# Kernel optimization log

Hardware: AMD Instinct MI355X
Metric: run time of the kernel (lower is better)

## Reference

```python
import jax, jax.numpy as jnp
import numpy as np

N, E, IN_DIM, OUT_DIM, HEADS = 50000, 800000, 128, 64, 2
NEG_SLOPE = 0.2  # DGL GATConv default leaky_relu slope


def setup_inputs() -> dict:
    key = jax.random.key(0)
    ks = jax.random.split(key, 11)
    p = lambda k, shape: jax.random.normal(k, shape, jnp.float32) * 0.05
    return dict(
        feature=jax.random.normal(ks[0], (N, IN_DIM), jnp.float32),
        src=jax.random.randint(ks[1], (E,), 0, N, jnp.int32),
        dst=jax.random.randint(ks[2], (E,), 0, N, jnp.int32),
        W1=p(ks[3], (IN_DIM, HEADS * OUT_DIM)),
        al1=p(ks[4], (HEADS, OUT_DIM)),
        ar1=p(ks[5], (HEADS, OUT_DIM)),
        b1=p(ks[6], (HEADS * OUT_DIM,)),
        W2=p(ks[7], (HEADS * OUT_DIM, OUT_DIM)),
        al2=p(ks[8], (1, OUT_DIM)),
        ar2=p(ks[9], (1, OUT_DIM)),
        b2=p(ks[10], (OUT_DIM,)),
    )


def gat_conv(x, W, al, ar, b, src, dst, n_nodes):
    # DGL GATConv (eval mode): fc -> per-node attn halves -> edge leaky_relu
    # -> edge-softmax grouped by dst -> scatter-weighted sum -> + bias
    H, D = al.shape
    h = (x @ W).reshape(n_nodes, H, D)               # [N,H,D]
    el = jnp.einsum('nhd,hd->nh', h, al)             # [N,H]
    er = jnp.einsum('nhd,hd->nh', h, ar)             # [N,H]
    e = jax.nn.leaky_relu(el[src] + er[dst], NEG_SLOPE)  # [E,H]
    m = jax.ops.segment_max(e, dst, num_segments=n_nodes)
    m = jnp.where(jnp.isfinite(m), m, 0.0)           # guard isolated dst nodes
    ex = jnp.exp(e - m[dst])                         # [E,H]
    s = jax.ops.segment_sum(ex, dst, num_segments=n_nodes)
    alpha = ex / s[dst]                              # edge-softmax weights
    out = jax.ops.segment_sum(alpha[:, :, None] * h[src], dst,
                              num_segments=n_nodes)  # [N,H,D]
    return out + b.reshape(H, D)


def reference(feature, src, dst, W1, al1, ar1, b1, W2, al2, ar2, b2):
    h1 = jax.nn.elu(gat_conv(feature, W1, al1, ar1, b1, src, dst, N))  # [N,2,D]
    h2 = gat_conv(h1.reshape(N, -1), W2, al2, ar2, b2, src, dst, N)    # [N,1,D]
    return (h1.mean(axis=1) + h2[:, 0, :]) * 0.5
```

## Files before the change

### kernel.cpp

```cpp
#include <hip/hip_runtime.h>
#include <hip/hip_fp16.h>
#include <math.h>

#define NNODES 50000
#define NEDGES 800000
#define CSR_STRIDE 48
#define NBUCKET 256
#define CHUNK 196
#define BCAP 4096
#define EPB 4096
#define NBLK_A ((NEDGES + EPB - 1) / EPB)
#define NBLK_G1 ((NNODES + 63) / 64)

typedef short bf16x8 __attribute__((ext_vector_type(8)));
typedef float f32x4  __attribute__((ext_vector_type(4)));

__device__ __forceinline__ unsigned bfpack(float a, float b) {
    unsigned ua = __float_as_uint(a), ub = __float_as_uint(b);
    ua = (ua + 0x7fffu + ((ua >> 16) & 1u)) >> 16;
    ub = (ub + 0x7fffu + ((ub >> 16) & 1u)) >> 16;
    return ua | (ub << 16);
}
__device__ __forceinline__ unsigned h2pack(float a, float b) {
    __half2 h = __floats2half2_rn(a, b);
    return *(unsigned*)&h;
}
__device__ __forceinline__ float hlo(unsigned u) {
    union { unsigned u; __half2 h; } c; c.u = u; return __half2float(c.h.x);
}
__device__ __forceinline__ float hhi(unsigned u) {
    union { unsigned u; __half2 h; } c; c.u = u; return __half2float(c.h.y);
}

__global__ __launch_bounds__(256) void prep_kernel(
    const int* __restrict__ src, const int* __restrict__ dst,
    int* __restrict__ bcnt, unsigned* __restrict__ bbuf,
    const float* __restrict__ W1, const float* __restrict__ W2,
    unsigned* __restrict__ W1t, unsigned* __restrict__ W2t) {
    const int tid = threadIdx.x;
    if (blockIdx.x < NBLK_A) {
        __shared__ int lcnt[NBUCKET];
        __shared__ int lcur[NBUCKET];
        lcnt[tid] = 0;
        __syncthreads();
        const int e0 = blockIdx.x * EPB;
        int e1 = e0 + EPB; if (e1 > NEDGES) e1 = NEDGES;
        for (int e = e0 + tid; e < e1; e += 256)
            atomicAdd(&lcnt[dst[e] / CHUNK], 1);
        __syncthreads();
        int c = lcnt[tid];
        int base = 0;
        if (c > 0) base = atomicAdd(&bcnt[tid], c);
        lcur[tid] = tid * BCAP + base;
        __syncthreads();
        for (int e = e0 + tid; e < e1; e += 256) {
            int d = dst[e], s = src[e];
            int b = d / CHUNK;
            int pos = atomicAdd(&lcur[b], 1);
            if (pos < (b + 1) * BCAP)
                bbuf[pos] = ((unsigned)(d - b * CHUNK) << 16) | (unsigned)s;
        }
    } else {
        int w = (blockIdx.x - NBLK_A) * 256 + tid;
        if (w < 8192) {
            int n = w >> 6, j = w & 63;
            W1t[w] = bfpack(W1[(2 * j) * 128 + n], W1[(2 * j + 1) * 128 + n]);
        } else {
            int w2 = w - 8192;
            int n = w2 >> 6, j = w2 & 63;
            W2t[w2] = bfpack(W2[(2 * j) * 64 + n], W2[(2 * j + 1) * 64 + n]);
        }
    }
}

__global__ __launch_bounds__(256) void build_gemm1_kernel(
    const int* __restrict__ bcnt, const unsigned* __restrict__ bbuf,
    int* __restrict__ deg, unsigned short* __restrict__ pcsr,
    const float* __restrict__ feat, const unsigned* __restrict__ Wt,
    const float* __restrict__ al, const float* __restrict__ ar,
    unsigned* __restrict__ h, float* __restrict__ el, float* __restrict__ er) {
    __shared__ uint4 smem4[(128 * 68 + 64 * 68) / 4];
    const int tid = threadIdx.x;

    if (blockIdx.x < NBUCKET) {
        int* ldeg = (int*)smem4;
        unsigned short* lcsr = (unsigned short*)(ldeg + CHUNK);
        const int b = blockIdx.x;
        const int n0 = b * CHUNK;
        int ncnt = NNODES - n0; if (ncnt > CHUNK) ncnt = CHUNK;
        for (int i = tid; i < CHUNK; i += 256) ldeg[i] = 0;
        __syncthreads();
        int cnt = bcnt[b]; if (cnt > BCAP) cnt = BCAP;
        const unsigned* bb = bbuf + (size_t)b * BCAP;
        for (int i = tid; i < cnt; i += 256) {
            unsigned e = bb[i];
            int ln = e >> 16;
            int p = atomicAdd(&ldeg[ln], 1);
            if (p < CSR_STRIDE) lcsr[ln * CSR_STRIDE + p] = (unsigned short)(e & 0xffffu);
        }
        __syncthreads();
        for (int i = tid; i < ncnt; i += 256) deg[n0 + i] = ldeg[i];
        const int nv = ncnt * (CSR_STRIDE / 8);
        uint4* d4 = (uint4*)(pcsr + (size_t)n0 * CSR_STRIDE);
        const uint4* s4 = (const uint4*)lcsr;
        for (int i = tid; i < nv; i += 256) d4[i] = s4[i];
        return;
    }

    unsigned* Wb = (unsigned*)smem4;
    unsigned* Ab = Wb + 128 * 68;
    const int n0 = (blockIdx.x - NBUCKET) * 64;

#pragma unroll
    for (int i = 0; i < 8; ++i) {
        int id = i * 256 + tid;
        int n = id >> 4, c = (id & 15) * 4;
        *(uint4*)&Wb[n * 68 + c] = *(const uint4*)&Wt[n * 64 + c];
    }
#pragma unroll
    for (int i = 0; i < 8; ++i) {
        int f = i * 256 + tid;
        int m = f >> 5, cf = (f & 31) * 4;
        float4 v = make_float4(0.f, 0.f, 0.f, 0.f);
        if (n0 + m < NNODES)
            v = *(const float4*)&feat[(size_t)(n0 + m) * 128 + cf];
        uint2 p = {bfpack(v.x, v.y), bfpack(v.z, v.w)};
        *(uint2*)&Ab[m * 68 + cf / 2] = p;
    }
    __syncthreads();

    const int w  = tid >> 6;
    const int l  = tid & 63;
    const int ml = l & 15;
    const int q  = l >> 4;
    f32x4 acc[8];
#pragma unroll
    for (int t = 0; t < 8; ++t) acc[t] = (f32x4){0.f, 0.f, 0.f, 0.f};

#pragma unroll
    for (int kc = 0; kc < 4; ++kc) {
        const int kw = kc * 16 + q * 4;
        uint4 a4 = *(uint4*)&Ab[(16 * w + ml) * 68 + kw];
        bf16x8 af = *(bf16x8*)&a4;
#pragma unroll
        for (int t = 0; t < 8; ++t) {
            uint4 b4 = *(uint4*)&Wb[(t * 16 + ml) * 68 + kw];
            bf16x8 bf = *(bf16x8*)&b4;
            acc[t] = __builtin_amdgcn_mfma_f32_16x16x32_bf16(af, bf, acc[t], 0, 0, 0);
        }
    }

    float av[8], rv[8];
#pragma unroll
    for (int t = 0; t < 8; ++t) { av[t] = al[t * 16 + ml]; rv[t] = ar[t * 16 + ml]; }

#pragma unroll
    for (int r = 0; r < 4; ++r) {
        const int node = n0 + 16 * w + q * 4 + r;
        float e0 = 0.f, e1 = 0.f, f0 = 0.f, f1 = 0.f;
#pragma unroll
        for (int t = 0; t < 8; ++t) {
            float v = acc[t][r];
            if (t < 4) { e0 = fmaf(v, av[t], e0); f0 = fmaf(v, rv[t], f0); }
            else       { e1 = fmaf(v, av[t], e1); f1 = fmaf(v, rv[t], f1); }
            float pv = __shfl_xor(v, 1);
            if ((ml & 1) == 0 && node < NNODES)
                h[(size_t)node * 64 + t * 8 + (ml >> 1)] = h2pack(v, pv);
        }
#pragma unroll
        for (int mm = 1; mm <= 8; mm <<= 1) {
            e0 += __shfl_xor(e0, mm); e1 += __shfl_xor(e1, mm);
            f0 += __shfl_xor(f0, mm); f1 += __shfl_xor(f1, mm);
        }
        if (ml == 0 && node < NNODES) {
            el[node * 2 + 0] = e0; el[node * 2 + 1] = e1;
            er[node * 2 + 0] = f0; er[node * 2 + 1] = f1;
        }
    }
}

__global__ __launch_bounds__(256) void gemm2_kernel(
    const unsigned* __restrict__ h1b, const unsigned* __restrict__ Wt,
    const float* __restrict__ al, const float* __restrict__ ar,
    unsigned* __restrict__ h2, float* __restrict__ el, float* __restrict__ er) {
    __shared__ unsigned Wb[64 * 68];
    __shared__ unsigned Ab[64 * 68];
    const int tid = threadIdx.x;
    const int n0  = blockIdx.x * 64;

#pragma unroll
    for (int i = 0; i < 4; ++i) {
        int id = i * 256 + tid;
        int n = id >> 4, c = (id & 15) * 4;
        *(uint4*)&Wb[n * 68 + c] = *(const uint4*)&Wt[n * 64 + c];
    }
#pragma unroll
    for (int i = 0; i < 4; ++i) {
        int id = i * 256 + tid;
        int m = id >> 4, c = (id & 15) * 4;
        uint4 v = make_uint4(0u, 0u, 0u, 0u);
        if (n0 + m < NNODES)
            v = *(const uint4*)&h1b[(size_t)(n0 + m) * 64 + c];
        *(uint4*)&Ab[m * 68 + c] = v;
    }
    __syncthreads();

    const int w  = tid >> 6;
    const int l  = tid & 63;
    const int ml = l & 15;
    const int q  = l >> 4;
    f32x4 acc[4];
#pragma unroll
    for (int t = 0; t < 4; ++t) acc[t] = (f32x4){0.f, 0.f, 0.f, 0.f};

#pragma unroll
    for (int kc = 0; kc < 4; ++kc) {
        const int kw = kc * 16 + q * 4;
        uint4 a4 = *(uint4*)&Ab[(16 * w + ml) * 68 + kw];
        bf16x8 af = *(bf16x8*)&a4;
#pragma unroll
        for (int t = 0; t < 4; ++t) {
            uint4 b4 = *(uint4*)&Wb[(t * 16 + ml) * 68 + kw];
            bf16x8 bf = *(bf16x8*)&b4;
            acc[t] = __builtin_amdgcn_mfma_f32_16x16x32_bf16(af, bf, acc[t], 0, 0, 0);
        }
    }

    float av[4], rv[4];
#pragma unroll
    for (int t = 0; t < 4; ++t) { av[t] = al[t * 16 + ml]; rv[t] = ar[t * 16 + ml]; }

#pragma unroll
    for (int r = 0; r < 4; ++r) {
        const int node = n0 + 16 * w + q * 4 + r;
        float e0 = 0.f, f0 = 0.f;
#pragma unroll
        for (int t = 0; t < 4; ++t) {
            float v = acc[t][r];
            e0 = fmaf(v, av[t], e0);
            f0 = fmaf(v, rv[t], f0);
            float pv = __shfl_xor(v, 1);
            if ((ml & 1) == 0 && node < NNODES)
                h2[(size_t)node * 32 + t * 8 + (ml >> 1)] = h2pack(v, pv);
        }
#pragma unroll
        for (int mm = 1; mm <= 8; mm <<= 1) {
            e0 += __shfl_xor(e0, mm);
            f0 += __shfl_xor(f0, mm);
        }
        if (ml == 0 && node < NNODES) { el[node] = e0; er[node] = f0; }
    }
}

#define FMA8(hv, A)                                              \
    a0r = fmaf(hlo(hv.x), A, a0r); a1r = fmaf(hhi(hv.x), A, a1r); \
    a2r = fmaf(hlo(hv.y), A, a2r); a3r = fmaf(hhi(hv.y), A, a3r); \
    a4r = fmaf(hlo(hv.z), A, a4r); a5r = fmaf(hhi(hv.z), A, a5r); \
    a6r = fmaf(hlo(hv.w), A, a6r); a7r = fmaf(hhi(hv.w), A, a7r);

__global__ __launch_bounds__(256) void aggregate1_kernel(
    const int* __restrict__ degv,
    const unsigned short* __restrict__ csr_src,
    const float* __restrict__ el, const float* __restrict__ er,
    const unsigned* __restrict__ hh, const float* __restrict__ bias,
    unsigned* __restrict__ h1b, float* __restrict__ hm) {
    const int wid  = (blockIdx.x * 256 + threadIdx.x) >> 6;
    const int lane = threadIdx.x & 63;
    const int g    = lane >> 4;
    const int l16  = lane & 15;
    const int gb   = g * 16;
    const int node = wid * 4 + g;
    if (node >= NNODES) return;
    const int row = node * CSR_STRIDE;
    int deg = degv[node];
    deg = deg < CSR_STRIDE ? deg : CSR_STRIDE;
    const float er0 = er[node * 2 + 0];
    const float er1 = er[node * 2 + 1];
    const bool hsel = (l16 >= 8);
    const unsigned* __restrict__ hq = hh + 4 * l16;

    int s0 = 0;
    if (l16 < deg) s0 = (int)csr_src[row + l16];

    uint4 hv[16];
#pragma unroll
    for (int j = 0; j < 16; ++j) {
        int s = __shfl(s0, gb + j);
        hv[j] = *(const uint4*)(hq + (size_t)s * 64);
    }

    float2 e2 = *(const float2*)&el[s0 * 2];
    float a = e2.x + er0; a = a > 0.f ? a : 0.2f * a;
    float b = e2.y + er1; b = b > 0.f ? b : 0.2f * b;
    float v0 = (l16 < deg) ? a : -1e30f;
    float v1 = (l16 < deg) ? b : -1e30f;
    float m0 = v0, m1 = v1;
    int   s1 = 0, s2 = 0;
    float va1 = -1e30f, vb1 = -1e30f, va2 = -1e30f, vb2 = -1e30f;
    if (deg > 16) {
        if (16 + l16 < deg) {
            s1 = (int)csr_src[row + 16 + l16];
            float2 ee = *(const float2*)&el[s1 * 2];
            float aa = ee.x + er0; va1 = aa > 0.f ? aa : 0.2f * aa;
            float bb = ee.y + er1; vb1 = bb > 0.f ? bb : 0.2f * bb;
            m0 = fmaxf(m0, va1); m1 = fmaxf(m1, vb1);
        }
        if (32 + l16 < deg) {
            s2 = (int)csr_src[row + 32 + l16];
            float2 ee = *(const float2*)&el[s2 * 2];
            float aa = ee.x + er0; va2 = aa > 0.f ? aa : 0.2f * aa;
            float bb = ee.y + er1; vb2 = bb > 0.f ? bb : 0.2f * bb;
            m0 = fmaxf(m0, va2); m1 = fmaxf(m1, vb2);
        }
    }
#pragma unroll
    for (int off = 8; off > 0; off >>= 1) {
        m0 = fmaxf(m0, __shfl_xor(m0, off));
        m1 = fmaxf(m1, __shfl_xor(m1, off));
    }
    float p0 = __expf(v0 - m0),  p1 = __expf(v1 - m1);
    float q0 = __expf(va1 - m0), q1 = __expf(vb1 - m1);
    float r0 = __expf(va2 - m0), r1 = __expf(vb2 - m1);
    float ssum0 = p0 + q0 + r0, ssum1 = p1 + q1 + r1;
#pragma unroll
    for (int off = 8; off > 0; off >>= 1) {
        ssum0 += __shfl_xor(ssum0, off);
        ssum1 += __shfl_xor(ssum1, off);
    }

    float a0r = 0.f, a1r = 0.f, a2r = 0.f, a3r = 0.f;
    float a4r = 0.f, a5r = 0.f, a6r = 0.f, a7r = 0.f;
#pragma unroll
    for (int j = 0; j < 16; ++j) {
        float x = __shfl(p0, gb + j);
        float y = __shfl(p1, gb + j);
        float A = hsel ? y : x;
        FMA8(hv[j], A)
    }
    if (deg > 16) {
        uint4 hw[16];
#pragma unroll
        for (int j = 0; j < 16; ++j) {
            int s = __shfl(s1, gb + j);
            hw[j] = *(const uint4*)(hq + (size_t)s * 64);
        }
#pragma unroll
        for (int j = 0; j < 16; ++j) {
            float x = __shfl(q0, gb + j);
            float y = __shfl(q1, gb + j);
            float A = hsel ? y : x;
            FMA8(hw[j], A)
        }
    }
    if (deg > 32) {
        uint4 hz[16];
#pragma unroll
        for (int j = 0; j < 16; ++j) {
            int s = __shfl(s2, gb + j);
            hz[j] = *(const uint4*)(hq + (size_t)s * 64);
        }
#pragma unroll
        for (int j = 0; j < 16; ++j) {
            float x = __shfl(r0, gb + j);
            float y = __shfl(r1, gb + j);
            float A = hsel ? y : x;
            FMA8(hz[j], A)
        }
    }

    const float ssum = hsel ? ssum1 : ssum0;
    const float inv  = (deg > 0) ? 1.f / ssum : 0.f;
    float4 b0 = *(const float4*)&bias[8 * l16];
    float4 b1 = *(const float4*)&bias[8 * l16 + 4];
    float o0 = fmaf(a0r, inv, b0.x), o1 = fmaf(a1r, inv, b0.y);
    float o2 = fmaf(a2r, inv, b0.z), o3 = fmaf(a3r, inv, b0.w);
    float o4 = fmaf(a4r, inv, b1.x), o5 = fmaf(a5r, inv, b1.y);
    float o6 = fmaf(a6r, inv, b1.z), o7 = fmaf(a7r, inv, b1.w);
    o0 = o0 > 0.f ? o0 : (__expf(o0) - 1.f);
    o1 = o1 > 0.f ? o1 : (__expf(o1) - 1.f);
    o2 = o2 > 0.f ? o2 : (__expf(o2) - 1.f);
    o3 = o3 > 0.f ? o3 : (__expf(o3) - 1.f);
    o4 = o4 > 0.f ? o4 : (__expf(o4) - 1.f);
    o5 = o5 > 0.f ? o5 : (__expf(o5) - 1.f);
    o6 = o6 > 0.f ? o6 : (__expf(o6) - 1.f);
    o7 = o7 > 0.f ? o7 : (__expf(o7) - 1.f);

    uint4 pk;
    pk.x = bfpack(o0, o1); pk.y = bfpack(o2, o3);
    pk.z = bfpack(o4, o5); pk.w = bfpack(o6, o7);
    *(uint4*)&h1b[(size_t)node * 64 + 4 * l16] = pk;

    float n0_ = 0.5f * (o0 + __shfl_xor(o0, 8));
    float n1_ = 0.5f * (o1 + __shfl_xor(o1, 8));
    float n2_ = 0.5f * (o2 + __shfl_xor(o2, 8));
    float n3_ = 0.5f * (o3 + __shfl_xor(o3, 8));
    float n4_ = 0.5f * (o4 + __shfl_xor(o4, 8));
    float n5_ = 0.5f * (o5 + __shfl_xor(o5, 8));
    float n6_ = 0.5f * (o6 + __shfl_xor(o6, 8));
    float n7_ = 0.5f * (o7 + __shfl_xor(o7, 8));
    if (l16 < 8) {
        *(float4*)&hm[(size_t)node * 64 + 8 * l16]     = make_float4(n0_, n1_, n2_, n3_);
        *(float4*)&hm[(size_t)node * 64 + 8 * l16 + 4] = make_float4(n4_, n5_, n6_, n7_);
    }
}

#define FMA4(hv, P)                                            \
    ax = fmaf(hlo(hv.x), P, ax); ay = fmaf(hhi(hv.x), P, ay);  \
    az = fmaf(hlo(hv.y), P, az); aw = fmaf(hhi(hv.y), P, aw);

__global__ __launch_bounds__(256) void aggregate2_kernel(
    const int* __restrict__ degv,
    const unsigned short* __restrict__ csr_src,
    const float* __restrict__ el, const float* __restrict__ er,
    const unsigned* __restrict__ hh, const float* __restrict__ bias,
    const float* __restrict__ hm, float* __restrict__ outp) {
    const int wid  = (blockIdx.x * 256 + threadIdx.x) >> 6;
    const int lane = threadIdx.x & 63;
    const int g    = lane >> 4;
    const int l16  = lane & 15;
    const int gb   = g * 16;
    const int node = wid * 4 + g;
    if (node >= NNODES) return;
    const int row = node * CSR_STRIDE;
    int deg = degv[node];
    deg = deg < CSR_STRIDE ? deg : CSR_STRIDE;
    const float erd = er[node];
    const unsigned* __restrict__ hq = hh + 2 * l16;

    int s0 = 0;
    if (l16 < deg) s0 = (int)csr_src[row + l16];

    uint2 hv[16];
#pragma unroll
    for (int j = 0; j < 16; ++j) {
        int s = __shfl(s0, gb + j);
        hv[j] = *(const uint2*)(hq + (size_t)s * 32);
    }

    float v = el[s0] + erd;
    v = v > 0.f ? v : 0.2f * v;
    float v0 = (l16 < deg) ? v : -1e30f;
    float m = v0;
    int   s1 = 0, s2 = 0;
    float va1 = -1e30f, va2 = -1e30f;
    if (deg > 16) {
        if (16 + l16 < deg) {
            s1 = (int)csr_src[row + 16 + l16];
            float vv = el[s1] + erd;
            va1 = vv > 0.f ? vv : 0.2f * vv;
            m = fmaxf(m, va1);
        }
        if (32 + l16 < deg) {
            s2 = (int)csr_src[row + 32 + l16];
            float vv = el[s2] + erd;
            va2 = vv > 0.f ? vv : 0.2f * vv;
            m = fmaxf(m, va2);
        }
    }
#pragma unroll
    for (int off = 8; off > 0; off >>= 1) m = fmaxf(m, __shfl_xor(m, off));
    float p0 = __expf(v0 - m);
    float q0 = __expf(va1 - m);
    float r0 = __expf(va2 - m);
    float ssum = p0 + q0 + r0;
#pragma unroll
    for (int off = 8; off > 0; off >>= 1) ssum += __shfl_xor(ssum, off);

    float ax = 0.f, ay = 0.f, az = 0.f, aw = 0.f;
#pragma unroll
    for (int j = 0; j < 16; ++j) {
        float p = __shfl(p0, gb + j);
        FMA4(hv[j], p)
    }
    if (deg > 16) {
        uint2 hw[16];
#pragma unroll
        for (int j = 0; j < 16; ++j) {
            int s = __shfl(s1, gb + j);
            hw[j] = *(const uint2*)(hq + (size_t)s * 32);
        }
#pragma unroll
        for (int j = 0; j < 16; ++j) {
            float p = __shfl(q0, gb + j);
            FMA4(hw[j], p)
        }
    }
    if (deg > 32) {
        uint2 hz[16];
#pragma unroll
        for (int j = 0; j < 16; ++j) {
            int s = __shfl(s2, gb + j);
            hz[j] = *(const uint2*)(hq + (size_t)s * 32);
        }
#pragma unroll
        for (int j = 0; j < 16; ++j) {
            float p = __shfl(r0, gb + j);
            FMA4(hz[j], p)
        }
    }

    float inv = (deg > 0) ? 1.f / ssum : 0.f;
    float4 hmv = *(const float4*)&hm[(size_t)node * 64 + 4 * l16];
    float4 bb  = *(const float4*)&bias[4 * l16];
    float o0 = (hmv.x + fmaf(ax, inv, bb.x)) * 0.5f;
    float o1 = (hmv.y + fmaf(ay, inv, bb.y)) * 0.5f;
    float o2 = (hmv.z + fmaf(az, inv, bb.z)) * 0.5f;
    float o3 = (hmv.w + fmaf(aw, inv, bb.w)) * 0.5f;
    *(float4*)&outp[(size_t)node * 64 + 4 * l16] = make_float4(o0, o1, o2, o3);
}


extern "C" void kernel_launch(void* const* d_in, const int* in_sizes, int n_in,
                              void* d_out, int out_size, void* d_ws, size_t ws_size,
                              hipStream_t stream) {
    const float* feat = (const float*)d_in[0];
    const int*   src  = (const int*)d_in[1];
    const int*   dst  = (const int*)d_in[2];
    const float* W1   = (const float*)d_in[3];
    const float* al1  = (const float*)d_in[4];
    const float* ar1  = (const float*)d_in[5];
    const float* b1   = (const float*)d_in[6];
    const float* W2   = (const float*)d_in[7];
    const float* al2  = (const float*)d_in[8];
    const float* ar2  = (const float*)d_in[9];
    const float* b2   = (const float*)d_in[10];
    float* out = (float*)d_out;

    int*            bcnt   = (int*)d_ws;
    int*            ideg   = bcnt + NBUCKET;
    unsigned*       iw1t   = (unsigned*)(ideg + NNODES);
    unsigned*       iw2t   = iw1t + 8192;
    unsigned short* pcsr   = (unsigned short*)(iw2t + 4096);
    unsigned*       gH1    = (unsigned*)(pcsr + (size_t)NNODES * CSR_STRIDE);
    unsigned*       gH2    = gH1;
    unsigned*       h1b    = gH1 + (size_t)NNODES * 64;
    unsigned*       bbuf   = h1b;
    float*          hmean  = (float*)(h1b + (size_t)NNODES * 64);
    float*          fEl1   = hmean + (size_t)NNODES * 64;
    float*          fEr1   = fEl1 + (size_t)NNODES * 2;
    float*          fEl2   = fEr1 + (size_t)NNODES * 2;
    float*          fEr2   = fEl2 + (size_t)NNODES;

    hipMemsetAsync(bcnt, 0, NBUCKET * sizeof(int), stream);
    prep_kernel<<<NBLK_A + 48, 256, 0, stream>>>(src, dst, bcnt, bbuf,
                                                 W1, W2, iw1t, iw2t);
    build_gemm1_kernel<<<NBUCKET + NBLK_G1, 256, 0, stream>>>(
        bcnt, bbuf, ideg, pcsr, feat, iw1t, al1, ar1, gH1, fEl1, fEr1);
    aggregate1_kernel<<<(NNODES + 15) / 16, 256, 0, stream>>>(
        ideg, pcsr, fEl1, fEr1, gH1, b1, h1b, hmean);
    gemm2_kernel<<<NBLK_G1, 256, 0, stream>>>(h1b, iw2t, al2, ar2,
                                              gH2, fEl2, fEr2);
    aggregate2_kernel<<<(NNODES + 15) / 16, 256, 0, stream>>>(
        ideg, pcsr, fEl2, fEr2, gH2, b2, hmean, out);
}
```

Baseline: 199.8 us.

## Split aggregate1 and overlap its tail with first gemm2 tiles; store head-mean in fp16

Aggregate1 is split at a node boundary. The second part now runs in a combined kernel alongside the gemm2 tiles for nodes already finished by the first part, and a final small gemm2 launch covers the remaining tiles. This hides the tail of aggregate1 and the inter-kernel gap behind gemm2 work. The head-mean buffer is also stored as fp16 instead of fp32, which halves its write and read traffic at some precision cost. gH2 gets its own buffer so the overlapped gemm2 writes do not alias gH1 while aggregate1 is still reading it.

```diff
diff --git a/kernel.cpp b/kernel.cpp
--- a/kernel.cpp
+++ b/kernel.cpp
@@ -11,6 +11,11 @@
 #define EPB 4096
 #define NBLK_A ((NEDGES + EPB - 1) / EPB)
 #define NBLK_G1 ((NNODES + 63) / 64)
+#define SPLIT 35712
+#define A1H0_BLKS (SPLIT / 16)
+#define A1H1_BLKS ((NNODES - SPLIT + 15) / 16)
+#define G2H0_TILES (SPLIT / 64)
+#define G2H1_TILES ((NNODES - SPLIT + 63) / 64)
 
 typedef short bf16x8 __attribute__((ext_vector_type(8)));
 typedef float f32x4  __attribute__((ext_vector_type(4)));
@@ -179,15 +184,11 @@
     }
 }
 
-__global__ __launch_bounds__(256) void gemm2_kernel(
+__device__ __forceinline__ void gemm2_work(
+    const int n0, const int tid, unsigned* Wb, unsigned* Ab,
     const unsigned* __restrict__ h1b, const unsigned* __restrict__ Wt,
     const float* __restrict__ al, const float* __restrict__ ar,
     unsigned* __restrict__ h2, float* __restrict__ el, float* __restrict__ er) {
-    __shared__ unsigned Wb[64 * 68];
-    __shared__ unsigned Ab[64 * 68];
-    const int tid = threadIdx.x;
-    const int n0  = blockIdx.x * 64;
-
 #pragma unroll
     for (int i = 0; i < 4; ++i) {
         int id = i * 256 + tid;
@@ -258,19 +259,15 @@
     a4r = fmaf(hlo(hv.z), A, a4r); a5r = fmaf(hhi(hv.z), A, a5r); \
     a6r = fmaf(hlo(hv.w), A, a6r); a7r = fmaf(hhi(hv.w), A, a7r);
 
-__global__ __launch_bounds__(256) void aggregate1_kernel(
-    const int* __restrict__ degv,
-    const unsigned short* __restrict__ csr_src,
+__device__ __forceinline__ void agg1_work(
+    const int node, const int lane,
+    const int* __restrict__ degv, const unsigned short* __restrict__ csr_src,
     const float* __restrict__ el, const float* __restrict__ er,
     const unsigned* __restrict__ hh, const float* __restrict__ bias,
-    unsigned* __restrict__ h1b, float* __restrict__ hm) {
-    const int wid  = (blockIdx.x * 256 + threadIdx.x) >> 6;
-    const int lane = threadIdx.x & 63;
+    unsigned* __restrict__ h1b, unsigned* __restrict__ hm16) {
     const int g    = lane >> 4;
     const int l16  = lane & 15;
     const int gb   = g * 16;
-    const int node = wid * 4 + g;
-    if (node >= NNODES) return;
     const int row = node * CSR_STRIDE;
     int deg = degv[node];
     deg = deg < CSR_STRIDE ? deg : CSR_STRIDE;
@@ -399,9 +396,57 @@
     float n6_ = 0.5f * (o6 + __shfl_xor(o6, 8));
     float n7_ = 0.5f * (o7 + __shfl_xor(o7, 8));
     if (l16 < 8) {
-        *(float4*)&hm[(size_t)node * 64 + 8 * l16]     = make_float4(n0_, n1_, n2_, n3_);
-        *(float4*)&hm[(size_t)node * 64 + 8 * l16 + 4] = make_float4(n4_, n5_, n6_, n7_);
-    }
+        uint4 hm;
+        hm.x = h2pack(n0_, n1_); hm.y = h2pack(n2_, n3_);
+        hm.z = h2pack(n4_, n5_); hm.w = h2pack(n6_, n7_);
+        *(uint4*)&hm16[(size_t)node * 32 + 4 * l16] = hm;
+    }
+}
+
+__global__ __launch_bounds__(256) void aggregate1_kernel(
+    const int nbase,
+    const int* __restrict__ degv, const unsigned short* __restrict__ csr_src,
+    const float* __restrict__ el, const float* __restrict__ er,
+    const unsigned* __restrict__ hh, const float* __restrict__ bias,
+    unsigned* __restrict__ h1b, unsigned* __restrict__ hm16) {
+    const int wid  = (blockIdx.x * 256 + threadIdx.x) >> 6;
+    const int lane = threadIdx.x & 63;
+    const int node = nbase + wid * 4 + (lane >> 4);
+    if (node >= NNODES) return;
+    agg1_work(node, lane, degv, csr_src, el, er, hh, bias, h1b, hm16);
+}
+
+__global__ __launch_bounds__(256) void agg1_gemm2_kernel(
+    const int* __restrict__ degv, const unsigned short* __restrict__ csr_src,
+    const float* __restrict__ el1, const float* __restrict__ er1,
+    const unsigned* __restrict__ hh, const float* __restrict__ b1,
+    unsigned* __restrict__ h1b, unsigned* __restrict__ hm16,
+    const unsigned* __restrict__ Wt2,
+    const float* __restrict__ al2, const float* __restrict__ ar2,
+    unsigned* __restrict__ h2, float* __restrict__ el2, float* __restrict__ er2) {
+    __shared__ unsigned smem[2 * 64 * 68];
+    const int tid = threadIdx.x;
+    if (blockIdx.x < A1H1_BLKS) {
+        const int wid  = (blockIdx.x * 256 + tid) >> 6;
+        const int lane = tid & 63;
+        const int node = SPLIT + wid * 4 + (lane >> 4);
+        if (node >= NNODES) return;
+        agg1_work(node, lane, degv, csr_src, el1, er1, hh, b1, h1b, hm16);
+    } else {
+        const int n0 = (blockIdx.x - A1H1_BLKS) * 64;
+        gemm2_work(n0, tid, smem, smem + 64 * 68, h1b, Wt2, al2, ar2,
+                   h2, el2, er2);
+    }
+}
+
+__global__ __launch_bounds__(256) void gemm2_kernel(
+    const int tbase,
+    const unsigned* __restrict__ h1b, const unsigned* __restrict__ Wt,
+    const float* __restrict__ al, const float* __restrict__ ar,
+    unsigned* __restrict__ h2, float* __restrict__ el, float* __restrict__ er) {
+    __shared__ unsigned smem[2 * 64 * 68];
+    gemm2_work((tbase + blockIdx.x) * 64, threadIdx.x, smem, smem + 64 * 68,
+               h1b, Wt, al, ar, h2, el, er);
 }
 
 #define FMA4(hv, P)                                            \
@@ -413,7 +458,7 @@
     const unsigned short* __restrict__ csr_src,
     const float* __restrict__ el, const float* __restrict__ er,
     const unsigned* __restrict__ hh, const float* __restrict__ bias,
-    const float* __restrict__ hm, float* __restrict__ outp) {
+    const unsigned* __restrict__ hm16, float* __restrict__ outp) {
     const int wid  = (blockIdx.x * 256 + threadIdx.x) >> 6;
     const int lane = threadIdx.x & 63;
     const int g    = lane >> 4;
@@ -500,12 +545,12 @@
     }
 
     float inv = (deg > 0) ? 1.f / ssum : 0.f;
-    float4 hmv = *(const float4*)&hm[(size_t)node * 64 + 4 * l16];
-    float4 bb  = *(const float4*)&bias[4 * l16];
-    float o0 = (hmv.x + fmaf(ax, inv, bb.x)) * 0.5f;
-    float o1 = (hmv.y + fmaf(ay, inv, bb.y)) * 0.5f;
-    float o2 = (hmv.z + fmaf(az, inv, bb.z)) * 0.5f;
-    float o3 = (hmv.w + fmaf(aw, inv, bb.w)) * 0.5f;
+    uint2 hm2 = *(const uint2*)&hm16[(size_t)node * 32 + 2 * l16];
+    float4 bb = *(const float4*)&bias[4 * l16];
+    float o0 = (hlo(hm2.x) + fmaf(ax, inv, bb.x)) * 0.5f;
+    float o1 = (hhi(hm2.x) + fmaf(ay, inv, bb.y)) * 0.5f;
+    float o2 = (hlo(hm2.y) + fmaf(az, inv, bb.z)) * 0.5f;
+    float o3 = (hhi(hm2.y) + fmaf(aw, inv, bb.w)) * 0.5f;
     *(float4*)&outp[(size_t)node * 64 + 4 * l16] = make_float4(o0, o1, o2, o3);
 }
 
@@ -532,11 +577,11 @@
     unsigned*       iw2t   = iw1t + 8192;
     unsigned short* pcsr   = (unsigned short*)(iw2t + 4096);
     unsigned*       gH1    = (unsigned*)(pcsr + (size_t)NNODES * CSR_STRIDE);
-    unsigned*       gH2    = gH1;
     unsigned*       h1b    = gH1 + (size_t)NNODES * 64;
     unsigned*       bbuf   = h1b;
-    float*          hmean  = (float*)(h1b + (size_t)NNODES * 64);
-    float*          fEl1   = hmean + (size_t)NNODES * 64;
+    unsigned*       gH2    = h1b + (size_t)NNODES * 64;
+    unsigned*       hm16   = gH2 + (size_t)NNODES * 32;
+    float*          fEl1   = (float*)(hm16 + (size_t)NNODES * 32);
     float*          fEr1   = fEl1 + (size_t)NNODES * 2;
     float*          fEl2   = fEr1 + (size_t)NNODES * 2;
     float*          fEr2   = fEl2 + (size_t)NNODES;
@@ -546,10 +591,13 @@
                                                  W1, W2, iw1t, iw2t);
     build_gemm1_kernel<<<NBUCKET + NBLK_G1, 256, 0, stream>>>(
         bcnt, bbuf, ideg, pcsr, feat, iw1t, al1, ar1, gH1, fEl1, fEr1);
-    aggregate1_kernel<<<(NNODES + 15) / 16, 256, 0, stream>>>(
-        ideg, pcsr, fEl1, fEr1, gH1, b1, h1b, hmean);
-    gemm2_kernel<<<NBLK_G1, 256, 0, stream>>>(h1b, iw2t, al2, ar2,
-                                              gH2, fEl2, fEr2);
+    aggregate1_kernel<<<A1H0_BLKS, 256, 0, stream>>>(
+        0, ideg, pcsr, fEl1, fEr1, gH1, b1, h1b, hm16);
+    agg1_gemm2_kernel<<<A1H1_BLKS + G2H0_TILES, 256, 0, stream>>>(
+        ideg, pcsr, fEl1, fEr1, gH1, b1, h1b, hm16,
+        iw2t, al2, ar2, gH2, fEl2, fEr2);
+    gemm2_kernel<<<G2H1_TILES, 256, 0, stream>>>(
+        G2H0_TILES, h1b, iw2t, al2, ar2, gH2, fEl2, fEr2);
     aggregate2_kernel<<<(NNODES + 15) / 16, 256, 0, stream>>>(
-        ideg, pcsr, fEl2, fEr2, gH2, b2, hmean, out);
-}
+        ideg, pcsr, fEl2, fEr2, gH2, b2, hm16, out);
+}
```

Result: slower. 206.6 us (+3.4%).
